# Kernel tuning notes

Measured on AMD Instinct MI355X. Metric: run time of the kernel, lower is better.

The kernel has to match this reference:

```python
import jax, jax.numpy as jnp
import numpy as np

N_MOTIF_PER_CLASS = 8
N_CLASS = 16
N_MOTIF = N_MOTIF_PER_CLASS * N_CLASS
TEMPERATURE = 0.2
TAU = 0.99
K2 = 32
EPS = 1e-4


def setup_inputs() -> dict:
    key = jax.random.key(0)
    k1, k2, k3 = jax.random.split(key, 3)
    N, H = 32768, 1024
    z = jax.random.normal(k1, (N, H), dtype=jnp.float32)
    Motif_Vector = jax.random.normal(k2, (N_MOTIF, H), dtype=jnp.float32)
    y = jax.random.randint(k3, (N,), 0, N_CLASS, dtype=jnp.int64)
    return {"z": z, "Motif_Vector": Motif_Vector, "y": y}


def euclidean_1(X, M):
    # squared euclidean distance via GEMM, then log-ratio similarity
    xp = X @ M.T                                     # [N, n_motif]
    distance = (-2.0 * xp
                + jnp.sum(X * X, axis=1, keepdims=True)
                + jnp.sum(M * M, axis=1)[None, :])
    similarity = jnp.log((distance + 1.0) / (distance + EPS))
    return similarity, distance


def reference(z, Motif_Vector, y):
    similarity, distance = euclidean_1(z, Motif_Vector)

    # mapping: motif j belongs to class j // n_motif_per_class
    motif_class = jnp.arange(N_MOTIF) // N_MOTIF_PER_CLASS   # [n_motif]
    true_motifs = (y[:, None] == motif_class[None, :])       # [N, n_motif]

    # contrastive loss (exact torch math: exp(sim/T), max over positives,
    # sum over negatives)
    sims = jnp.exp(similarity / TEMPERATURE)
    sim_pos = jnp.max(jnp.where(true_motifs, sims, -jnp.inf), axis=1)
    sim_neg_sum = jnp.sum(jnp.where(true_motifs, 0.0, sims), axis=1)
    loss = -jnp.mean(jnp.log(sim_pos / (sim_neg_sum + sim_pos)))

    # update_motif (update_type='topk', weighted_mean=False):
    # torch passes `distance` into filter_similar_graph and argsorts
    # descending, i.e. selects the K2 LARGEST distances among same-class
    # samples (faithful to source).
    masked = jnp.where(true_motifs.T, distance.T, -jnp.inf)  # [n_motif, N]
    _, idx = jax.lax.top_k(masked, K2)                       # [n_motif, K2]
    selected = z[idx]                                        # [n_motif, K2, H]
    new_motif = jnp.mean(selected, axis=1)                   # weights = 1/K2
    new_M = TAU * Motif_Vector + (1.0 - TAU) * new_motif

    return loss, new_M
```

## Files before the change

kernel.cpp:

```cpp
#include <hip/hip_runtime.h>
#include <cstdint>
#include <cmath>

#define NROWS 32768
#define HD    1024
#define NMOT  128
#define NCLS  16
#define KSEL  32
#define EPSV  1e-4f

typedef __attribute__((ext_vector_type(4))) float  f32x4;
typedef __attribute__((ext_vector_type(8))) __bf16 bf16x8;
typedef __attribute__((ext_vector_type(4))) __bf16 bf16x4;
typedef unsigned long long u64;

#define WS_LP   0
#define WS_MN   512
#define WS_MVBF 1024
#define WS_S1K  66560
#define WS_CD   197632
#define CAPC    256

static __device__ __forceinline__ float dot4(float4 v) {
    return v.x * v.x + v.y * v.y + v.z * v.z + v.w * v.w;
}

static __device__ __forceinline__ bf16x4 cvt4(float4 v) {
    bf16x4 t;
    t[0] = (__bf16)v.x; t[1] = (__bf16)v.y; t[2] = (__bf16)v.z; t[3] = (__bf16)v.w;
    return t;
}

static __device__ __forceinline__ bf16x8 cvt8(float4 a, float4 b) {
    bf16x8 t;
    t[0] = (__bf16)a.x; t[1] = (__bf16)a.y; t[2] = (__bf16)a.z; t[3] = (__bf16)a.w;
    t[4] = (__bf16)b.x; t[5] = (__bf16)b.y; t[6] = (__bf16)b.z; t[7] = (__bf16)b.w;
    return t;
}

static __device__ __forceinline__ void gl16(const void* g, void* l) {
    __builtin_amdgcn_global_load_lds(
        (const __attribute__((address_space(1))) void*)g,
        (__attribute__((address_space(3))) void*)l, 16, 0, 0);
}

static __device__ __forceinline__ u64 pack_key(float v, int idx) {
    unsigned int b = __float_as_uint(v);
    unsigned int mo = (b & 0x80000000u) ? ~b : (b | 0x80000000u);
    unsigned int khi = ~mo;
    return ((u64)khi << 32) | (unsigned int)idx;
}

__global__ __launch_bounds__(256) void prep_k(const float* __restrict__ mv,
                                              float* __restrict__ mn,
                                              __bf16* __restrict__ mvbf) {
    const int b = blockIdx.x;
    const int tid = threadIdx.x;
    const int k = tid * 4;
    float4 v = *(const float4*)&mv[(size_t)b * HD + k];
    *(bf16x4*)&mvbf[(size_t)b * HD + k] = cvt4(v);
    float s = dot4(v);
#pragma unroll
    for (int o = 1; o < 64; o <<= 1) s += __shfl_xor(s, o, 64);
    __shared__ float red[4];
    if ((tid & 63) == 0) red[tid >> 6] = s;
    __syncthreads();
    if (tid == 0) mn[b] = red[0] + red[1] + red[2] + red[3];
}

#define BM 64
#define BK 32
#define NS (HD / BK)

__global__ __launch_bounds__(256, 2) void gemm_fused(
    const float* __restrict__ z, const __bf16* __restrict__ mvbf,
    const float* __restrict__ mn, float* __restrict__ cd,
    const int* __restrict__ y, float* __restrict__ lossP) {
    __shared__ __align__(16) __bf16 Bs[4][4096];
    __shared__ float redw[4];

    const int tid  = threadIdx.x;
    const int lane = tid & 63;
    const int wid  = tid >> 6;
    const int l15  = lane & 15;
    const int quad = lane >> 4;
    const int row0 = blockIdx.x * BM;
    const int myrow = row0 + wid * 16 + l15;

    const float* zrow = z + (size_t)myrow * HD + quad * 8;

    const int g1 = tid, g2 = tid + 256;
    const int r1 = g1 >> 2, r2 = g2 >> 2;
    const int q1 = (g1 & 3) ^ ((r1 >> 1) & 3);
    const int q2 = (g2 & 3) ^ ((r2 >> 1) & 3);
    const __bf16* bsrc1 = mvbf + r1 * HD + q1 * 8;
    const __bf16* bsrc2 = mvbf + r2 * HD + q2 * 8;
    char* bs = (char*)Bs;
    const int bofs = l15 * 64 + ((quad ^ ((l15 >> 1) & 3)) << 4);

    float mcv[8];
#pragma unroll
    for (int j = 0; j < 8; ++j) mcv[j] = mn[j * 16 + l15];
    const int yv = y[myrow];

    f32x4 acc[8];
#pragma unroll
    for (int j = 0; j < 8; ++j) acc[j] = (f32x4){0.f, 0.f, 0.f, 0.f};
    float zsq = 0.f;
    float4 ra[2][2];

    gl16(bsrc1,      bs + 0 * 8192 + wid * 1024);
    gl16(bsrc2,      bs + 0 * 8192 + 4096 + wid * 1024);
    gl16(bsrc1 + BK, bs + 1 * 8192 + wid * 1024);
    gl16(bsrc2 + BK, bs + 1 * 8192 + 4096 + wid * 1024);
    ra[0][0] = *(const float4*)(zrow);
    ra[0][1] = *(const float4*)(zrow + 4);
    ra[1][0] = *(const float4*)(zrow + BK);
    ra[1][1] = *(const float4*)(zrow + BK + 4);
    __builtin_amdgcn_sched_barrier(0);
    asm volatile("s_waitcnt vmcnt(6)" ::: "memory");
    __builtin_amdgcn_s_barrier();
    asm volatile("" ::: "memory");
    __builtin_amdgcn_sched_barrier(0);

    for (int it = 0; it < NS / 4; ++it) {
#pragma unroll
        for (int u = 0; u < 4; ++u) {
            const int kt = it * 4 + u;
            const int slot = u & 1;
            bf16x8 bfr[8];
#pragma unroll
            for (int j = 0; j < 8; ++j)
                bfr[j] = *(const bf16x8*)(bs + u * 8192 + j * 1024 + bofs);
            if (kt + 2 < NS) {
                char* d = bs + ((u + 2) & 3) * 8192 + wid * 1024;
                gl16(bsrc1 + (kt + 2) * BK, d);
                gl16(bsrc2 + (kt + 2) * BK, d + 4096);
            }
            bf16x8 af = cvt8(ra[slot][0], ra[slot][1]);
            zsq += dot4(ra[slot][0]) + dot4(ra[slot][1]);
            if (kt + 2 < NS) {
                ra[slot][0] = *(const float4*)(zrow + (kt + 2) * BK);
                ra[slot][1] = *(const float4*)(zrow + (kt + 2) * BK + 4);
            }
#pragma unroll
            for (int j = 0; j < 8; ++j)
                acc[j] = __builtin_amdgcn_mfma_f32_16x16x32_bf16(
                    af, bfr[j], acc[j], 0, 0, 0);
            if (kt + 2 < NS) {
                __builtin_amdgcn_sched_barrier(0);
                asm volatile("s_waitcnt vmcnt(4) lgkmcnt(0)" ::: "memory");
                __builtin_amdgcn_s_barrier();
                asm volatile("" ::: "memory");
                __builtin_amdgcn_sched_barrier(0);
            } else if (kt + 1 < NS) {
                __builtin_amdgcn_sched_barrier(0);
                asm volatile("s_waitcnt vmcnt(2) lgkmcnt(0)" ::: "memory");
                __builtin_amdgcn_s_barrier();
                asm volatile("" ::: "memory");
                __builtin_amdgcn_sched_barrier(0);
            }
        }
    }

    zsq += __shfl_xor(zsq, 16, 64);
    zsq += __shfl_xor(zsq, 32, 64);

    float znv[4]; int rcls[4];
#pragma unroll
    for (int reg = 0; reg < 4; ++reg) {
        znv[reg]  = __shfl(zsq, quad * 4 + reg, 64);
        rcls[reg] = __shfl(yv,  quad * 4 + reg, 64);
    }
    float pm[4], ns[4];
#pragma unroll
    for (int reg = 0; reg < 4; ++reg) { pm[reg] = 0.f; ns[reg] = 0.f; }

#pragma unroll
    for (int j = 0; j < 8; ++j) {
        const int c = j * 16 + l15;
        const float mc = mcv[j];
        const int ccls = c >> 3;
#pragma unroll
        for (int reg = 0; reg < 4; ++reg) {
            float d = znv[reg] + mc - 2.f * acc[j][reg];
            float r = (d + 1.0f) * __builtin_amdgcn_rcpf(d + EPSV);
            float r2 = r * r;
            float s = r2 * r2 * r;
            if (ccls == rcls[reg]) {
                pm[reg] = fmaxf(pm[reg], s);
                const int row = row0 + wid * 16 + quad * 4 + reg;
                cd[(size_t)row * 8 + (c & 7)] = d;
            } else {
                ns[reg] += s;
            }
        }
    }
#pragma unroll
    for (int o = 1; o < 16; o <<= 1)
#pragma unroll
        for (int reg = 0; reg < 4; ++reg) {
            pm[reg] = fmaxf(pm[reg], __shfl_xor(pm[reg], o, 64));
            ns[reg] += __shfl_xor(ns[reg], o, 64);
        }
    float li = 0.f;
    if (l15 == 0) {
#pragma unroll
        for (int reg = 0; reg < 4; ++reg)
            li += logf((ns[reg] + pm[reg]) / pm[reg]);
    }
    li += __shfl_xor(li, 16, 64);
    li += __shfl_xor(li, 32, 64);
    if (lane == 0) redw[wid] = li;
    __syncthreads();
    if (tid == 0) lossP[blockIdx.x] = redw[0] + redw[1] + redw[2] + redw[3];
}

__global__ __launch_bounds__(256) void sel1_k(const int* __restrict__ y,
                                              const float* __restrict__ cd,
                                              u64* __restrict__ s1k) {
    __shared__ u64 keys[256];
    __shared__ int clist[CAPC];
    __shared__ int cnt;

    const int bid = blockIdx.x;
    const int j = bid >> 4, chunk = bid & 15;
    const int cls = j >> 3, m8 = j & 7;
    const int tid = threadIdx.x;
    const int lane = tid & 63;

    if (tid == 0) cnt = 0;
    __syncthreads();
    const int base = chunk * 2048;
#pragma unroll
    for (int t = 0; t < 8; ++t) {
        const int i = base + t * 256 + tid;
        const bool pred = (y[i] == cls);
        const u64 m = __ballot(pred);
        int wbase = 0;
        if (lane == 0 && m) wbase = atomicAdd(&cnt, (int)__popcll(m));
        wbase = __shfl(wbase, 0, 64);
        if (pred) {
            const int p = wbase + (int)__popcll(m & ((1ull << lane) - 1ull));
            if (p < CAPC) clist[p] = i;
        }
    }
    __syncthreads();
    const int n = cnt < CAPC ? cnt : CAPC;

    u64 key = ~0ull;
    if (tid < n) {
        const int idx = clist[tid];
        key = pack_key(cd[(size_t)idx * 8 + m8], idx);
    }
    keys[tid] = key;
    __syncthreads();

    for (int k = 2; k <= 256; k <<= 1) {
        for (int jj = k >> 1; jj > 0; jj >>= 1) {
            if (tid < 128) {
                const int i  = ((tid & ~(jj - 1)) << 1) | (tid & (jj - 1));
                const int ix = i | jj;
                const u64 A = keys[i], B = keys[ix];
                const bool up = ((i & k) == 0);
                if ((A > B) == up) { keys[i] = B; keys[ix] = A; }
            }
            __syncthreads();
        }
    }
    if (tid < KSEL) s1k[(size_t)j * 512 + chunk * KSEL + tid] = keys[tid];
}

__global__ __launch_bounds__(256) void merge_k(
    const float* __restrict__ z, const float* __restrict__ mv,
    const u64* __restrict__ s1k, const float* __restrict__ lossP,
    float* __restrict__ out) {
    __shared__ u64 keys[512];
    __shared__ int sel[KSEL];
    __shared__ float redf[4];

    const int b = blockIdx.x;
    const int j = b >> 2, q = b & 3;
    const int tid = threadIdx.x;
    const int lane = tid & 63;
    const int wave = tid >> 6;

    if (b == 0) {
        float s = lossP[tid] + lossP[tid + 256];
#pragma unroll
        for (int o = 1; o < 64; o <<= 1) s += __shfl_xor(s, o, 64);
        if (lane == 0) redf[wave] = s;
        __syncthreads();
        if (tid == 0)
            out[0] = (redf[0] + redf[1] + redf[2] + redf[3]) * (1.0f / NROWS);
    }

    keys[tid]       = s1k[(size_t)j * 512 + tid];
    keys[tid + 256] = s1k[(size_t)j * 512 + 256 + tid];
    __syncthreads();

    for (int k = 2; k <= 512; k <<= 1) {
        for (int jj = k >> 1; jj > 0; jj >>= 1) {
            const int i  = ((tid & ~(jj - 1)) << 1) | (tid & (jj - 1));
            const int ix = i | jj;
            const u64 A = keys[i], B = keys[ix];
            const bool up = ((i & k) == 0);
            if ((A > B) == up) { keys[i] = B; keys[ix] = A; }
            __syncthreads();
        }
    }
    if (tid < KSEL) sel[tid] = (int)(keys[tid] & 0xFFFFFFFFu);
    __syncthreads();

    const int h = q * 256 + tid;
    float s = 0.f;
#pragma unroll 8
    for (int r = 0; r < KSEL; ++r) s += z[(size_t)sel[r] * HD + h];
    out[1 + (size_t)j * HD + h] =
        0.99f * mv[(size_t)j * HD + h] + 0.01f * (s * (1.0f / KSEL));
}

extern "C" void kernel_launch(void* const* d_in, const int* in_sizes, int n_in,
                              void* d_out, int out_size, void* d_ws, size_t ws_size,
                              hipStream_t stream) {
    const float* z  = (const float*)d_in[0];
    const float* mv = (const float*)d_in[1];
    const int*   y  = (const int*)d_in[2];
    float* out = (float*)d_out;
    float* wsf = (float*)d_ws;
    float*  lossP = wsf + WS_LP;
    float*  mn    = wsf + WS_MN;
    __bf16* mvbf  = (__bf16*)(wsf + WS_MVBF);
    u64*    s1k   = (u64*)(wsf + WS_S1K);
    float*  cd    = wsf + WS_CD;

    hipLaunchKernelGGL(prep_k,     dim3(NMOT),      dim3(256), 0, stream,
                       mv, mn, mvbf);
    hipLaunchKernelGGL(gemm_fused, dim3(NROWS / BM), dim3(256), 0, stream,
                       z, mvbf, mn, cd, y, lossP);
    hipLaunchKernelGGL(sel1_k,     dim3(NMOT * 16), dim3(256), 0, stream,
                       y, cd, s1k);
    hipLaunchKernelGGL(merge_k,    dim3(NMOT * 4),  dim3(256), 0, stream,
                       z, mv, s1k, lossP, out);
}
```

Baseline: 232.5 us.

## Fuse four kernels into one cooperative kernel with grid syncs

Merges the prep, GEMM+loss, per-chunk top-k and merge kernels into a single cooperative persistent kernel of 512 blocks, separated by grid-wide syncs, with a fallback to four phase launches if the cooperative launch fails. It also restructures the first top-k stage so each wave handles one chunk (512 blocks instead of 2048), using per-wave ballot compaction without shared atomics. The aim is to remove kernel launch gaps and tail effects between stages. The cost is grid-sync overhead and a single shared-memory and register footprint across all phases, which could lower GEMM occupancy.

```diff
diff --git a/kernel.cpp b/kernel.cpp
--- a/kernel.cpp
+++ b/kernel.cpp
@@ -1,6 +1,9 @@
 #include <hip/hip_runtime.h>
+#include <hip/hip_cooperative_groups.h>
 #include <cstdint>
 #include <cmath>
+
+namespace cg = cooperative_groups;
 
 #define NROWS 32768
 #define HD    1024
@@ -51,273 +54,281 @@
     return ((u64)khi << 32) | (unsigned int)idx;
 }
 
-__global__ __launch_bounds__(256) void prep_k(const float* __restrict__ mv,
-                                              float* __restrict__ mn,
-                                              __bf16* __restrict__ mvbf) {
-    const int b = blockIdx.x;
-    const int tid = threadIdx.x;
-    const int k = tid * 4;
-    float4 v = *(const float4*)&mv[(size_t)b * HD + k];
-    *(bf16x4*)&mvbf[(size_t)b * HD + k] = cvt4(v);
-    float s = dot4(v);
-#pragma unroll
-    for (int o = 1; o < 64; o <<= 1) s += __shfl_xor(s, o, 64);
-    __shared__ float red[4];
-    if ((tid & 63) == 0) red[tid >> 6] = s;
-    __syncthreads();
-    if (tid == 0) mn[b] = red[0] + red[1] + red[2] + red[3];
-}
-
 #define BM 64
 #define BK 32
 #define NS (HD / BK)
 
-__global__ __launch_bounds__(256, 2) void gemm_fused(
-    const float* __restrict__ z, const __bf16* __restrict__ mvbf,
-    const float* __restrict__ mn, float* __restrict__ cd,
-    const int* __restrict__ y, float* __restrict__ lossP) {
-    __shared__ __align__(16) __bf16 Bs[4][4096];
-    __shared__ float redw[4];
+__global__ __launch_bounds__(256, 2) void fused_all(
+    const float* __restrict__ z, const float* __restrict__ mv,
+    const int* __restrict__ y, float* __restrict__ out,
+    float* __restrict__ wsf, int phase) {
+
+    __shared__ __align__(16) char smem[32800];
+
+    float*  lossP = wsf + WS_LP;
+    float*  mn    = wsf + WS_MN;
+    __bf16* mvbf  = (__bf16*)(wsf + WS_MVBF);
+    u64*    s1k   = (u64*)(wsf + WS_S1K);
+    float*  cd    = wsf + WS_CD;
 
     const int tid  = threadIdx.x;
     const int lane = tid & 63;
     const int wid  = tid >> 6;
-    const int l15  = lane & 15;
-    const int quad = lane >> 4;
-    const int row0 = blockIdx.x * BM;
-    const int myrow = row0 + wid * 16 + l15;
-
-    const float* zrow = z + (size_t)myrow * HD + quad * 8;
-
-    const int g1 = tid, g2 = tid + 256;
-    const int r1 = g1 >> 2, r2 = g2 >> 2;
-    const int q1 = (g1 & 3) ^ ((r1 >> 1) & 3);
-    const int q2 = (g2 & 3) ^ ((r2 >> 1) & 3);
-    const __bf16* bsrc1 = mvbf + r1 * HD + q1 * 8;
-    const __bf16* bsrc2 = mvbf + r2 * HD + q2 * 8;
-    char* bs = (char*)Bs;
-    const int bofs = l15 * 64 + ((quad ^ ((l15 >> 1) & 3)) << 4);
-
-    float mcv[8];
-#pragma unroll
-    for (int j = 0; j < 8; ++j) mcv[j] = mn[j * 16 + l15];
-    const int yv = y[myrow];
-
-    f32x4 acc[8];
-#pragma unroll
-    for (int j = 0; j < 8; ++j) acc[j] = (f32x4){0.f, 0.f, 0.f, 0.f};
-    float zsq = 0.f;
-    float4 ra[2][2];
-
-    gl16(bsrc1,      bs + 0 * 8192 + wid * 1024);
-    gl16(bsrc2,      bs + 0 * 8192 + 4096 + wid * 1024);
-    gl16(bsrc1 + BK, bs + 1 * 8192 + wid * 1024);
-    gl16(bsrc2 + BK, bs + 1 * 8192 + 4096 + wid * 1024);
-    ra[0][0] = *(const float4*)(zrow);
-    ra[0][1] = *(const float4*)(zrow + 4);
-    ra[1][0] = *(const float4*)(zrow + BK);
-    ra[1][1] = *(const float4*)(zrow + BK + 4);
-    __builtin_amdgcn_sched_barrier(0);
-    asm volatile("s_waitcnt vmcnt(6)" ::: "memory");
-    __builtin_amdgcn_s_barrier();
-    asm volatile("" ::: "memory");
-    __builtin_amdgcn_sched_barrier(0);
-
-    for (int it = 0; it < NS / 4; ++it) {
-#pragma unroll
-        for (int u = 0; u < 4; ++u) {
-            const int kt = it * 4 + u;
-            const int slot = u & 1;
-            bf16x8 bfr[8];
-#pragma unroll
-            for (int j = 0; j < 8; ++j)
-                bfr[j] = *(const bf16x8*)(bs + u * 8192 + j * 1024 + bofs);
-            if (kt + 2 < NS) {
-                char* d = bs + ((u + 2) & 3) * 8192 + wid * 1024;
-                gl16(bsrc1 + (kt + 2) * BK, d);
-                gl16(bsrc2 + (kt + 2) * BK, d + 4096);
-            }
-            bf16x8 af = cvt8(ra[slot][0], ra[slot][1]);
-            zsq += dot4(ra[slot][0]) + dot4(ra[slot][1]);
-            if (kt + 2 < NS) {
-                ra[slot][0] = *(const float4*)(zrow + (kt + 2) * BK);
-                ra[slot][1] = *(const float4*)(zrow + (kt + 2) * BK + 4);
-            }
-#pragma unroll
-            for (int j = 0; j < 8; ++j)
-                acc[j] = __builtin_amdgcn_mfma_f32_16x16x32_bf16(
-                    af, bfr[j], acc[j], 0, 0, 0);
-            if (kt + 2 < NS) {
-                __builtin_amdgcn_sched_barrier(0);
-                asm volatile("s_waitcnt vmcnt(4) lgkmcnt(0)" ::: "memory");
-                __builtin_amdgcn_s_barrier();
-                asm volatile("" ::: "memory");
-                __builtin_amdgcn_sched_barrier(0);
-            } else if (kt + 1 < NS) {
-                __builtin_amdgcn_sched_barrier(0);
-                asm volatile("s_waitcnt vmcnt(2) lgkmcnt(0)" ::: "memory");
-                __builtin_amdgcn_s_barrier();
-                asm volatile("" ::: "memory");
-                __builtin_amdgcn_sched_barrier(0);
-            }
-        }
-    }
-
-    zsq += __shfl_xor(zsq, 16, 64);
-    zsq += __shfl_xor(zsq, 32, 64);
-
-    float znv[4]; int rcls[4];
-#pragma unroll
-    for (int reg = 0; reg < 4; ++reg) {
-        znv[reg]  = __shfl(zsq, quad * 4 + reg, 64);
-        rcls[reg] = __shfl(yv,  quad * 4 + reg, 64);
-    }
-    float pm[4], ns[4];
-#pragma unroll
-    for (int reg = 0; reg < 4; ++reg) { pm[reg] = 0.f; ns[reg] = 0.f; }
-
-#pragma unroll
-    for (int j = 0; j < 8; ++j) {
-        const int c = j * 16 + l15;
-        const float mc = mcv[j];
-        const int ccls = c >> 3;
+    const int b    = blockIdx.x;
+    const bool all = (phase < 0);
+
+    if (all || phase == 0) {
+        if (b < NMOT) {
+            float* red = (float*)smem;
+            const int k = tid * 4;
+            float4 v = *(const float4*)&mv[(size_t)b * HD + k];
+            *(bf16x4*)&mvbf[(size_t)b * HD + k] = cvt4(v);
+            float s = dot4(v);
+#pragma unroll
+            for (int o = 1; o < 64; o <<= 1) s += __shfl_xor(s, o, 64);
+            if (lane == 0) red[wid] = s;
+            __syncthreads();
+            if (tid == 0) mn[b] = red[0] + red[1] + red[2] + red[3];
+        }
+    }
+    if (all) cg::this_grid().sync();
+
+    if (all || phase == 1) {
+        char*  bs   = smem;
+        float* redw = (float*)(smem + 32768);
+
+        const int l15  = lane & 15;
+        const int quad = lane >> 4;
+        const int row0 = b * BM;
+        const int myrow = row0 + wid * 16 + l15;
+
+        const float* zrow = z + (size_t)myrow * HD + quad * 8;
+
+        const int g1 = tid, g2 = tid + 256;
+        const int r1 = g1 >> 2, r2 = g2 >> 2;
+        const int q1 = (g1 & 3) ^ ((r1 >> 1) & 3);
+        const int q2 = (g2 & 3) ^ ((r2 >> 1) & 3);
+        const __bf16* bsrc1 = mvbf + r1 * HD + q1 * 8;
+        const __bf16* bsrc2 = mvbf + r2 * HD + q2 * 8;
+        const int bofs = l15 * 64 + ((quad ^ ((l15 >> 1) & 3)) << 4);
+
+        float mcv[8];
+#pragma unroll
+        for (int j = 0; j < 8; ++j) mcv[j] = mn[j * 16 + l15];
+        const int yv = y[myrow];
+
+        f32x4 acc[8];
+#pragma unroll
+        for (int j = 0; j < 8; ++j) acc[j] = (f32x4){0.f, 0.f, 0.f, 0.f};
+        float zsq = 0.f;
+        float4 ra[2][2];
+
+        gl16(bsrc1,      bs + 0 * 8192 + wid * 1024);
+        gl16(bsrc2,      bs + 0 * 8192 + 4096 + wid * 1024);
+        gl16(bsrc1 + BK, bs + 1 * 8192 + wid * 1024);
+        gl16(bsrc2 + BK, bs + 1 * 8192 + 4096 + wid * 1024);
+        ra[0][0] = *(const float4*)(zrow);
+        ra[0][1] = *(const float4*)(zrow + 4);
+        ra[1][0] = *(const float4*)(zrow + BK);
+        ra[1][1] = *(const float4*)(zrow + BK + 4);
+        __builtin_amdgcn_sched_barrier(0);
+        asm volatile("s_waitcnt vmcnt(6)" ::: "memory");
+        __builtin_amdgcn_s_barrier();
+        asm volatile("" ::: "memory");
+        __builtin_amdgcn_sched_barrier(0);
+
+        for (int it = 0; it < NS / 4; ++it) {
+#pragma unroll
+            for (int u = 0; u < 4; ++u) {
+                const int kt = it * 4 + u;
+                const int slot = u & 1;
+                bf16x8 bfr[8];
+#pragma unroll
+                for (int j = 0; j < 8; ++j)
+                    bfr[j] = *(const bf16x8*)(bs + u * 8192 + j * 1024 + bofs);
+                if (kt + 2 < NS) {
+                    char* d = bs + ((u + 2) & 3) * 8192 + wid * 1024;
+                    gl16(bsrc1 + (kt + 2) * BK, d);
+                    gl16(bsrc2 + (kt + 2) * BK, d + 4096);
+                }
+                bf16x8 af = cvt8(ra[slot][0], ra[slot][1]);
+                zsq += dot4(ra[slot][0]) + dot4(ra[slot][1]);
+                if (kt + 2 < NS) {
+                    ra[slot][0] = *(const float4*)(zrow + (kt + 2) * BK);
+                    ra[slot][1] = *(const float4*)(zrow + (kt + 2) * BK + 4);
+                }
+#pragma unroll
+                for (int j = 0; j < 8; ++j)
+                    acc[j] = __builtin_amdgcn_mfma_f32_16x16x32_bf16(
+                        af, bfr[j], acc[j], 0, 0, 0);
+                if (kt + 2 < NS) {
+                    __builtin_amdgcn_sched_barrier(0);
+                    asm volatile("s_waitcnt vmcnt(4) lgkmcnt(0)" ::: "memory");
+                    __builtin_amdgcn_s_barrier();
+                    asm volatile("" ::: "memory");
+                    __builtin_amdgcn_sched_barrier(0);
+                } else if (kt + 1 < NS) {
+                    __builtin_amdgcn_sched_barrier(0);
+                    asm volatile("s_waitcnt vmcnt(2) lgkmcnt(0)" ::: "memory");
+                    __builtin_amdgcn_s_barrier();
+                    asm volatile("" ::: "memory");
+                    __builtin_amdgcn_sched_barrier(0);
+                }
+            }
+        }
+
+        zsq += __shfl_xor(zsq, 16, 64);
+        zsq += __shfl_xor(zsq, 32, 64);
+
+        float znv[4]; int rcls[4];
 #pragma unroll
         for (int reg = 0; reg < 4; ++reg) {
-            float d = znv[reg] + mc - 2.f * acc[j][reg];
-            float r = (d + 1.0f) * __builtin_amdgcn_rcpf(d + EPSV);
-            float r2 = r * r;
-            float s = r2 * r2 * r;
-            if (ccls == rcls[reg]) {
-                pm[reg] = fmaxf(pm[reg], s);
-                const int row = row0 + wid * 16 + quad * 4 + reg;
-                cd[(size_t)row * 8 + (c & 7)] = d;
-            } else {
-                ns[reg] += s;
-            }
-        }
-    }
-#pragma unroll
-    for (int o = 1; o < 16; o <<= 1)
-#pragma unroll
-        for (int reg = 0; reg < 4; ++reg) {
-            pm[reg] = fmaxf(pm[reg], __shfl_xor(pm[reg], o, 64));
-            ns[reg] += __shfl_xor(ns[reg], o, 64);
-        }
-    float li = 0.f;
-    if (l15 == 0) {
-#pragma unroll
-        for (int reg = 0; reg < 4; ++reg)
-            li += logf((ns[reg] + pm[reg]) / pm[reg]);
-    }
-    li += __shfl_xor(li, 16, 64);
-    li += __shfl_xor(li, 32, 64);
-    if (lane == 0) redw[wid] = li;
-    __syncthreads();
-    if (tid == 0) lossP[blockIdx.x] = redw[0] + redw[1] + redw[2] + redw[3];
-}
-
-__global__ __launch_bounds__(256) void sel1_k(const int* __restrict__ y,
-                                              const float* __restrict__ cd,
-                                              u64* __restrict__ s1k) {
-    __shared__ u64 keys[256];
-    __shared__ int clist[CAPC];
-    __shared__ int cnt;
-
-    const int bid = blockIdx.x;
-    const int j = bid >> 4, chunk = bid & 15;
-    const int cls = j >> 3, m8 = j & 7;
-    const int tid = threadIdx.x;
-    const int lane = tid & 63;
-
-    if (tid == 0) cnt = 0;
-    __syncthreads();
-    const int base = chunk * 2048;
-#pragma unroll
-    for (int t = 0; t < 8; ++t) {
-        const int i = base + t * 256 + tid;
-        const bool pred = (y[i] == cls);
-        const u64 m = __ballot(pred);
-        int wbase = 0;
-        if (lane == 0 && m) wbase = atomicAdd(&cnt, (int)__popcll(m));
-        wbase = __shfl(wbase, 0, 64);
-        if (pred) {
-            const int p = wbase + (int)__popcll(m & ((1ull << lane) - 1ull));
-            if (p < CAPC) clist[p] = i;
-        }
-    }
-    __syncthreads();
-    const int n = cnt < CAPC ? cnt : CAPC;
-
-    u64 key = ~0ull;
-    if (tid < n) {
-        const int idx = clist[tid];
-        key = pack_key(cd[(size_t)idx * 8 + m8], idx);
-    }
-    keys[tid] = key;
-    __syncthreads();
-
-    for (int k = 2; k <= 256; k <<= 1) {
-        for (int jj = k >> 1; jj > 0; jj >>= 1) {
-            if (tid < 128) {
+            znv[reg]  = __shfl(zsq, quad * 4 + reg, 64);
+            rcls[reg] = __shfl(yv,  quad * 4 + reg, 64);
+        }
+        float pm[4], ns[4];
+#pragma unroll
+        for (int reg = 0; reg < 4; ++reg) { pm[reg] = 0.f; ns[reg] = 0.f; }
+
+#pragma unroll
+        for (int j = 0; j < 8; ++j) {
+            const int c = j * 16 + l15;
+            const float mc = mcv[j];
+            const int ccls = c >> 3;
+#pragma unroll
+            for (int reg = 0; reg < 4; ++reg) {
+                float d = znv[reg] + mc - 2.f * acc[j][reg];
+                float r = (d + 1.0f) * __builtin_amdgcn_rcpf(d + EPSV);
+                float r2 = r * r;
+                float s = r2 * r2 * r;
+                if (ccls == rcls[reg]) {
+                    pm[reg] = fmaxf(pm[reg], s);
+                    const int row = row0 + wid * 16 + quad * 4 + reg;
+                    cd[(size_t)row * 8 + (c & 7)] = d;
+                } else {
+                    ns[reg] += s;
+                }
+            }
+        }
+#pragma unroll
+        for (int o = 1; o < 16; o <<= 1)
+#pragma unroll
+            for (int reg = 0; reg < 4; ++reg) {
+                pm[reg] = fmaxf(pm[reg], __shfl_xor(pm[reg], o, 64));
+                ns[reg] += __shfl_xor(ns[reg], o, 64);
+            }
+        float li = 0.f;
+        if (l15 == 0) {
+#pragma unroll
+            for (int reg = 0; reg < 4; ++reg)
+                li += logf((ns[reg] + pm[reg]) / pm[reg]);
+        }
+        li += __shfl_xor(li, 16, 64);
+        li += __shfl_xor(li, 32, 64);
+        if (lane == 0) redw[wid] = li;
+        __syncthreads();
+        if (tid == 0) lossP[b] = redw[0] + redw[1] + redw[2] + redw[3];
+    }
+    if (all) cg::this_grid().sync();
+
+    if (all || phase == 2) {
+        u64 (*keys4)[256]  = (u64(*)[256])smem;
+        int (*clist4)[CAPC] = (int(*)[CAPC])(smem + 8192);
+
+        const int j2 = b >> 2, g2 = b & 3;
+        const int cls2 = j2 >> 3, m8 = j2 & 7;
+        const int chunk = g2 * 4 + wid;
+        const int base = chunk * 2048;
+
+        __syncthreads();
+
+        int cnt = 0;
+#pragma unroll
+        for (int t = 0; t < 32; ++t) {
+            const int i = base + t * 64 + lane;
+            const bool pred = (y[i] == cls2);
+            const u64 m = __ballot(pred);
+            if (pred) {
+                const int p = cnt + (int)__popcll(m & ((1ull << lane) - 1ull));
+                if (p < CAPC) clist4[wid][p] = i;
+            }
+            cnt += (int)__popcll(m);
+        }
+        const int n = cnt < CAPC ? cnt : CAPC;
+        __syncthreads();
+#pragma unroll
+        for (int t = 0; t < 4; ++t) {
+            const int l = t * 64 + lane;
+            u64 key = ~0ull;
+            if (l < n) {
+                const int idx = clist4[wid][l];
+                key = pack_key(cd[(size_t)idx * 8 + m8], idx);
+            }
+            keys4[wid][l] = key;
+        }
+        __syncthreads();
+        for (int k = 2; k <= 256; k <<= 1) {
+            for (int jj = k >> 1; jj > 0; jj >>= 1) {
+#pragma unroll
+                for (int t = 0; t < 2; ++t) {
+                    const int pid = t * 64 + lane;
+                    const int i  = ((pid & ~(jj - 1)) << 1) | (pid & (jj - 1));
+                    const int ix = i | jj;
+                    const u64 A = keys4[wid][i], B = keys4[wid][ix];
+                    const bool up = ((i & k) == 0);
+                    if ((A > B) == up) { keys4[wid][i] = B; keys4[wid][ix] = A; }
+                }
+                __syncthreads();
+            }
+        }
+        if (lane < KSEL)
+            s1k[(size_t)j2 * 512 + chunk * KSEL + lane] = keys4[wid][lane];
+    }
+    if (all) cg::this_grid().sync();
+
+    if (all || phase == 3) {
+        u64*   keysM = (u64*)smem;
+        int*   sel   = (int*)(smem + 4096);
+        float* redf  = (float*)(smem + 4096 + 128);
+
+        const int j3 = b >> 2, q = b & 3;
+
+        __syncthreads();
+
+        if (b == 0) {
+            float s = lossP[tid] + lossP[tid + 256];
+#pragma unroll
+            for (int o = 1; o < 64; o <<= 1) s += __shfl_xor(s, o, 64);
+            if (lane == 0) redf[wid] = s;
+            __syncthreads();
+            if (tid == 0)
+                out[0] = (redf[0] + redf[1] + redf[2] + redf[3]) * (1.0f / NROWS);
+        }
+
+        keysM[tid]       = s1k[(size_t)j3 * 512 + tid];
+        keysM[tid + 256] = s1k[(size_t)j3 * 512 + 256 + tid];
+        __syncthreads();
+
+        for (int k = 2; k <= 512; k <<= 1) {
+            for (int jj = k >> 1; jj > 0; jj >>= 1) {
                 const int i  = ((tid & ~(jj - 1)) << 1) | (tid & (jj - 1));
                 const int ix = i | jj;
-                const u64 A = keys[i], B = keys[ix];
+                const u64 A = keysM[i], B = keysM[ix];
                 const bool up = ((i & k) == 0);
-                if ((A > B) == up) { keys[i] = B; keys[ix] = A; }
-            }
-            __syncthreads();
-        }
-    }
-    if (tid < KSEL) s1k[(size_t)j * 512 + chunk * KSEL + tid] = keys[tid];
-}
-
-__global__ __launch_bounds__(256) void merge_k(
-    const float* __restrict__ z, const float* __restrict__ mv,
-    const u64* __restrict__ s1k, const float* __restrict__ lossP,
-    float* __restrict__ out) {
-    __shared__ u64 keys[512];
-    __shared__ int sel[KSEL];
-    __shared__ float redf[4];
-
-    const int b = blockIdx.x;
-    const int j = b >> 2, q = b & 3;
-    const int tid = threadIdx.x;
-    const int lane = tid & 63;
-    const int wave = tid >> 6;
-
-    if (b == 0) {
-        float s = lossP[tid] + lossP[tid + 256];
-#pragma unroll
-        for (int o = 1; o < 64; o <<= 1) s += __shfl_xor(s, o, 64);
-        if (lane == 0) redf[wave] = s;
-        __syncthreads();
-        if (tid == 0)
-            out[0] = (redf[0] + redf[1] + redf[2] + redf[3]) * (1.0f / NROWS);
-    }
-
-    keys[tid]       = s1k[(size_t)j * 512 + tid];
-    keys[tid + 256] = s1k[(size_t)j * 512 + 256 + tid];
-    __syncthreads();
-
-    for (int k = 2; k <= 512; k <<= 1) {
-        for (int jj = k >> 1; jj > 0; jj >>= 1) {
-            const int i  = ((tid & ~(jj - 1)) << 1) | (tid & (jj - 1));
-            const int ix = i | jj;
-            const u64 A = keys[i], B = keys[ix];
-            const bool up = ((i & k) == 0);
-            if ((A > B) == up) { keys[i] = B; keys[ix] = A; }
-            __syncthreads();
-        }
-    }
-    if (tid < KSEL) sel[tid] = (int)(keys[tid] & 0xFFFFFFFFu);
-    __syncthreads();
-
-    const int h = q * 256 + tid;
-    float s = 0.f;
+                if ((A > B) == up) { keysM[i] = B; keysM[ix] = A; }
+                __syncthreads();
+            }
+        }
+        if (tid < KSEL) sel[tid] = (int)(keysM[tid] & 0xFFFFFFFFu);
+        __syncthreads();
+
+        const int h = q * 256 + tid;
+        float s = 0.f;
 #pragma unroll 8
-    for (int r = 0; r < KSEL; ++r) s += z[(size_t)sel[r] * HD + h];
-    out[1 + (size_t)j * HD + h] =
-        0.99f * mv[(size_t)j * HD + h] + 0.01f * (s * (1.0f / KSEL));
+        for (int r = 0; r < KSEL; ++r) s += z[(size_t)sel[r] * HD + h];
+        out[1 + (size_t)j3 * HD + h] =
+            0.99f * mv[(size_t)j3 * HD + h] + 0.01f * (s * (1.0f / KSEL));
+    }
 }
 
 extern "C" void kernel_launch(void* const* d_in, const int* in_sizes, int n_in,
@@ -328,18 +339,27 @@
     const int*   y  = (const int*)d_in[2];
     float* out = (float*)d_out;
     float* wsf = (float*)d_ws;
-    float*  lossP = wsf + WS_LP;
-    float*  mn    = wsf + WS_MN;
-    __bf16* mvbf  = (__bf16*)(wsf + WS_MVBF);
-    u64*    s1k   = (u64*)(wsf + WS_S1K);
-    float*  cd    = wsf + WS_CD;
-
-    hipLaunchKernelGGL(prep_k,     dim3(NMOT),      dim3(256), 0, stream,
-                       mv, mn, mvbf);
-    hipLaunchKernelGGL(gemm_fused, dim3(NROWS / BM), dim3(256), 0, stream,
-                       z, mvbf, mn, cd, y, lossP);
-    hipLaunchKernelGGL(sel1_k,     dim3(NMOT * 16), dim3(256), 0, stream,
-                       y, cd, s1k);
-    hipLaunchKernelGGL(merge_k,    dim3(NMOT * 4),  dim3(256), 0, stream,
-                       z, mv, s1k, lossP, out);
-}
+
+    int phase = -1;
+    void* kargs[6];
+    kargs[0] = (void*)&z;
+    kargs[1] = (void*)&mv;
+    kargs[2] = (void*)&y;
+    kargs[3] = (void*)&out;
+    kargs[4] = (void*)&wsf;
+    kargs[5] = (void*)&phase;
+
+    hipError_t e = hipLaunchCooperativeKernel(
+        (const void*)fused_all, dim3(512), dim3(256), kargs, 0, stream);
+    if (e != hipSuccess) {
+        (void)hipGetLastError();
+        hipLaunchKernelGGL(fused_all, dim3(NMOT), dim3(256), 0, stream,
+                           z, mv, y, out, wsf, 0);
+        hipLaunchKernelGGL(fused_all, dim3(512), dim3(256), 0, stream,
+                           z, mv, y, out, wsf, 1);
+        hipLaunchKernelGGL(fused_all, dim3(512), dim3(256), 0, stream,
+                           z, mv, y, out, wsf, 2);
+        hipLaunchKernelGGL(fused_all, dim3(512), dim3(256), 0, stream,
+                           z, mv, y, out, wsf, 3);
+    }
+}
```

Result: slower. 406.6 us (+74.9%).

## Load motif B fragments directly from global into registers, dropping LDS staging

Applied to the files above, without the earlier changes.

The GEMM no longer stages the bf16 motif matrix through a 4-slot LDS ring filled by global_load_lds, and it drops the per-step barriers. Each lane now loads its own bf16x8 B fragments straight from global memory (cache-resident, 256 KB) into a double-buffered register array. This removes LDS traffic and block-wide synchronisation. The cost is more VGPRs, redundant per-wave global loads of B, and a dependence on L2/L1 hit rates.

```diff
diff --git a/kernel.cpp b/kernel.cpp
--- a/kernel.cpp
+++ b/kernel.cpp
@@ -36,12 +36,6 @@
     t[0] = (__bf16)a.x; t[1] = (__bf16)a.y; t[2] = (__bf16)a.z; t[3] = (__bf16)a.w;
     t[4] = (__bf16)b.x; t[5] = (__bf16)b.y; t[6] = (__bf16)b.z; t[7] = (__bf16)b.w;
     return t;
-}
-
-static __device__ __forceinline__ void gl16(const void* g, void* l) {
-    __builtin_amdgcn_global_load_lds(
-        (const __attribute__((address_space(1))) void*)g,
-        (__attribute__((address_space(3))) void*)l, 16, 0, 0);
 }
 
 static __device__ __forceinline__ u64 pack_key(float v, int idx) {
@@ -76,7 +70,6 @@
     const float* __restrict__ z, const __bf16* __restrict__ mvbf,
     const float* __restrict__ mn, float* __restrict__ cd,
     const int* __restrict__ y, float* __restrict__ lossP) {
-    __shared__ __align__(16) __bf16 Bs[4][4096];
     __shared__ float redw[4];
 
     const int tid  = threadIdx.x;
@@ -89,14 +82,10 @@
 
     const float* zrow = z + (size_t)myrow * HD + quad * 8;
 
-    const int g1 = tid, g2 = tid + 256;
-    const int r1 = g1 >> 2, r2 = g2 >> 2;
-    const int q1 = (g1 & 3) ^ ((r1 >> 1) & 3);
-    const int q2 = (g2 & 3) ^ ((r2 >> 1) & 3);
-    const __bf16* bsrc1 = mvbf + r1 * HD + q1 * 8;
-    const __bf16* bsrc2 = mvbf + r2 * HD + q2 * 8;
-    char* bs = (char*)Bs;
-    const int bofs = l15 * 64 + ((quad ^ ((l15 >> 1) & 3)) << 4);
+    const __bf16* bbase[8];
+#pragma unroll
+    for (int j = 0; j < 8; ++j)
+        bbase[j] = mvbf + (size_t)(j * 16 + l15) * HD + quad * 8;
 
     float mcv[8];
 #pragma unroll
@@ -107,60 +96,34 @@
 #pragma unroll
     for (int j = 0; j < 8; ++j) acc[j] = (f32x4){0.f, 0.f, 0.f, 0.f};
     float zsq = 0.f;
+
+    bf16x8 rb[2][8];
     float4 ra[2][2];
-
-    gl16(bsrc1,      bs + 0 * 8192 + wid * 1024);
-    gl16(bsrc2,      bs + 0 * 8192 + 4096 + wid * 1024);
-    gl16(bsrc1 + BK, bs + 1 * 8192 + wid * 1024);
-    gl16(bsrc2 + BK, bs + 1 * 8192 + 4096 + wid * 1024);
+#pragma unroll
+    for (int j = 0; j < 8; ++j) rb[0][j] = *(const bf16x8*)(bbase[j]);
     ra[0][0] = *(const float4*)(zrow);
     ra[0][1] = *(const float4*)(zrow + 4);
     ra[1][0] = *(const float4*)(zrow + BK);
     ra[1][1] = *(const float4*)(zrow + BK + 4);
-    __builtin_amdgcn_sched_barrier(0);
-    asm volatile("s_waitcnt vmcnt(6)" ::: "memory");
-    __builtin_amdgcn_s_barrier();
-    asm volatile("" ::: "memory");
-    __builtin_amdgcn_sched_barrier(0);
-
-    for (int it = 0; it < NS / 4; ++it) {
-#pragma unroll
-        for (int u = 0; u < 4; ++u) {
-            const int kt = it * 4 + u;
-            const int slot = u & 1;
-            bf16x8 bfr[8];
+
+#pragma unroll
+    for (int kt = 0; kt < NS; ++kt) {
+        const int s = kt & 1;
+        bf16x8 af = cvt8(ra[s][0], ra[s][1]);
+        zsq += dot4(ra[s][0]) + dot4(ra[s][1]);
+        if (kt + 2 < NS) {
+            ra[s][0] = *(const float4*)(zrow + (kt + 2) * BK);
+            ra[s][1] = *(const float4*)(zrow + (kt + 2) * BK + 4);
+        }
+        if (kt + 1 < NS) {
 #pragma unroll
             for (int j = 0; j < 8; ++j)
-                bfr[j] = *(const bf16x8*)(bs + u * 8192 + j * 1024 + bofs);
-            if (kt + 2 < NS) {
-                char* d = bs + ((u + 2) & 3) * 8192 + wid * 1024;
-                gl16(bsrc1 + (kt + 2) * BK, d);
-                gl16(bsrc2 + (kt + 2) * BK, d + 4096);
-            }
-            bf16x8 af = cvt8(ra[slot][0], ra[slot][1]);
-            zsq += dot4(ra[slot][0]) + dot4(ra[slot][1]);
-            if (kt + 2 < NS) {
-                ra[slot][0] = *(const float4*)(zrow + (kt + 2) * BK);
-                ra[slot][1] = *(const float4*)(zrow + (kt + 2) * BK + 4);
-            }
-#pragma unroll
-            for (int j = 0; j < 8; ++j)
-                acc[j] = __builtin_amdgcn_mfma_f32_16x16x32_bf16(
-                    af, bfr[j], acc[j], 0, 0, 0);
-            if (kt + 2 < NS) {
-                __builtin_amdgcn_sched_barrier(0);
-                asm volatile("s_waitcnt vmcnt(4) lgkmcnt(0)" ::: "memory");
-                __builtin_amdgcn_s_barrier();
-                asm volatile("" ::: "memory");
-                __builtin_amdgcn_sched_barrier(0);
-            } else if (kt + 1 < NS) {
-                __builtin_amdgcn_sched_barrier(0);
-                asm volatile("s_waitcnt vmcnt(2) lgkmcnt(0)" ::: "memory");
-                __builtin_amdgcn_s_barrier();
-                asm volatile("" ::: "memory");
-                __builtin_amdgcn_sched_barrier(0);
-            }
-        }
+                rb[s ^ 1][j] = *(const bf16x8*)(bbase[j] + (kt + 1) * BK);
+        }
+#pragma unroll
+        for (int j = 0; j < 8; ++j)
+            acc[j] = __builtin_amdgcn_mfma_f32_16x16x32_bf16(
+                af, rb[s][j], acc[j], 0, 0, 0);
     }
 
     zsq += __shfl_xor(zsq, 16, 64);
@@ -334,12 +297,12 @@
     u64*    s1k   = (u64*)(wsf + WS_S1K);
     float*  cd    = wsf + WS_CD;
 
-    hipLaunchKernelGGL(prep_k,     dim3(NMOT),      dim3(256), 0, stream,
+    hipLaunchKernelGGL(prep_k,     dim3(NMOT),       dim3(256), 0, stream,
                        mv, mn, mvbf);
     hipLaunchKernelGGL(gemm_fused, dim3(NROWS / BM), dim3(256), 0, stream,
                        z, mvbf, mn, cd, y, lossP);
-    hipLaunchKernelGGL(sel1_k,     dim3(NMOT * 16), dim3(256), 0, stream,
+    hipLaunchKernelGGL(sel1_k,     dim3(NMOT * 16),  dim3(256), 0, stream,
                        y, cd, s1k);
-    hipLaunchKernelGGL(merge_k,    dim3(NMOT * 4),  dim3(256), 0, stream,
+    hipLaunchKernelGGL(merge_k,    dim3(NMOT * 4),   dim3(256), 0, stream,
                        z, mv, s1k, lossP, out);
 }
```

Measured after the change: 263.3 us. 1.13x slower.
